# Performance work log

Hardware: AMD Instinct MI355X
Metric: run time of the kernel (lower is better)

## Reference

```python
import jax, jax.numpy as jnp
import numpy as np

NUM_HEADS = 8
EPS = 1e-9


def setup_inputs() -> dict:
    key = jax.random.key(0)
    ks = jax.random.split(key, 8)
    B, N, D = 2, 2048, 512
    s = 1.0 / np.sqrt(D)
    x = jax.random.normal(ks[0], (B, N, D), dtype=jnp.float32)
    adjacency = jax.random.uniform(ks[1], (B, N, N), dtype=jnp.float32)
    # Linear weights stored as (in, out) so application is x @ W + b
    W_q = jax.random.normal(ks[2], (D, D), dtype=jnp.float32) * s
    W_k = jax.random.normal(ks[3], (D, D), dtype=jnp.float32) * s
    W_v = jax.random.normal(ks[4], (D, D), dtype=jnp.float32) * s
    b_q = jnp.zeros((D,), jnp.float32)
    b_k = jnp.zeros((D,), jnp.float32)
    b_v = jnp.zeros((D,), jnp.float32)
    # soul_gate: Linear(2D -> 1); weight stored as flat (2D,), bias scalar
    w_g = jax.random.normal(ks[5], (2 * D,), dtype=jnp.float32) * (1.0 / np.sqrt(2 * D))
    b_g = jnp.zeros((), jnp.float32)
    return {"x": x, "adjacency": adjacency, "W_q": W_q, "b_q": b_q,
            "W_k": W_k, "b_k": b_k, "W_v": W_v, "b_v": b_v,
            "w_g": w_g, "b_g": b_g}


def reference(x, adjacency, W_q, b_q, W_k, b_k, W_v, b_v, w_g, b_g):
    B, N, D = x.shape
    H = NUM_HEADS
    hd = D // H
    Q = (x @ W_q + b_q).reshape(B, N, H, hd)
    K = (x @ W_k + b_k).reshape(B, N, H, hd)
    V = (x @ W_v + b_v).reshape(B, N, H, hd)
    scores = jnp.einsum('bihd,bjhd->bhij', Q, K) / jnp.sqrt(jnp.float32(hd))
    # soul_gate(cat[x_i, x_j]) is linear, so it decomposes exactly:
    # bias[b,i,j] = x[b,i]@w_g[:D] + x[b,j]@w_g[D:] + b_g  (same math, no (B,N,N,2D) tensor)
    a = x @ w_g[:D]          # (B, N) contribution of x_i
    c = x @ w_g[D:]          # (B, N) contribution of x_j
    soul_bias = a[:, :, None] + c[:, None, :] + b_g   # (B, N, N)
    scores = scores + (soul_bias + jnp.log(adjacency + EPS))[:, None, :, :]
    attn = jax.nn.softmax(scores, axis=-1)            # (B, H, N, N)
    out = jnp.einsum('bhij,bjhd->bihd', attn, V).reshape(B, N, D)
    return out + x
```

## Files before the change

kernel.cpp:

```cpp
#include <hip/hip_runtime.h>
#include <hip/hip_bf16.h>

typedef __bf16 bf16x8 __attribute__((ext_vector_type(8)));
typedef float f32x4 __attribute__((ext_vector_type(4)));
typedef unsigned short u16x8 __attribute__((ext_vector_type(8)));

#define LOG2E 1.44269504f

__device__ __forceinline__ unsigned short f2bu(float f) {
    __hip_bfloat16 h = __float2bfloat16(f);
    unsigned short u;
    __builtin_memcpy(&u, &h, 2);
    return u;
}

__device__ __forceinline__ float fexp2(float x) {
#if __has_builtin(__builtin_amdgcn_exp2f)
    return __builtin_amdgcn_exp2f(x);
#else
    return __expf(x * 0.69314718f);
#endif
}

__device__ __forceinline__ float bu2f(unsigned short u) {
    unsigned int v = ((unsigned int)u) << 16;
    float f;
    __builtin_memcpy(&f, &v, 4);
    return f;
}

#define GLDS16(gp, lp) __builtin_amdgcn_global_load_lds( \
    (const __attribute__((address_space(1))) unsigned int*)(gp), \
    (__attribute__((address_space(3))) unsigned int*)(lp), 16, 0, 0)

#define OFF_QS  0u
#define OFF_KB  4194304u
#define OFF_VT  8388608u
#define OFF_CV  12582912u
#define OFF_MP  12648448u
#define OFF_PO  29425664u
#define OFF_PL  37814272u
#define OFF_XB  OFF_MP
#define OFF_WT  (OFF_MP + 4194304u)

__global__ void k_prepwt(const float* __restrict__ x, const float* __restrict__ wg,
                         const float* __restrict__ w0, const float* __restrict__ w1,
                         const float* __restrict__ w2,
                         unsigned short* __restrict__ xb, float* __restrict__ cv2,
                         unsigned short* __restrict__ wt) {
    if (blockIdx.x < 1024) {
        int row = blockIdx.x * 4 + (threadIdx.x >> 6);
        int l = threadIdx.x & 63;
        const float4* xr = reinterpret_cast<const float4*>(x + (size_t)row * 512);
        float4 a = xr[l * 2], b2 = xr[l * 2 + 1];
        ushort4 o0, o1;
        o0.x = f2bu(a.x);  o0.y = f2bu(a.y);  o0.z = f2bu(a.z);  o0.w = f2bu(a.w);
        o1.x = f2bu(b2.x); o1.y = f2bu(b2.y); o1.z = f2bu(b2.z); o1.w = f2bu(b2.w);
        ushort4* dst = reinterpret_cast<ushort4*>(xb + (size_t)row * 512);
        dst[l * 2] = o0; dst[l * 2 + 1] = o1;
        const float4* wr = reinterpret_cast<const float4*>(wg + 512);
        float4 g0 = wr[l * 2], g1 = wr[l * 2 + 1];
        float s = a.x * g0.x + a.y * g0.y + a.z * g0.z + a.w * g0.w
                + b2.x * g1.x + b2.y * g1.y + b2.z * g1.z + b2.w * g1.w;
#pragma unroll
        for (int off = 32; off >= 1; off >>= 1) s += __shfl_xor(s, off, 64);
        if (l == 0) cv2[row] = fexp2((s - 8.0f) * LOG2E);
    } else {
        int bid2 = blockIdx.x - 1024;
        int z = bid2 >> 6, yy = bid2 & 63;
        int k0 = (yy >> 3) * 64, n0 = (yy & 7) * 64;
        const float* W = (z == 0) ? w0 : ((z == 1) ? w1 : w2);
        __shared__ float T[64][65];
        int c = threadIdx.x & 63, r0 = threadIdx.x >> 6;
#pragma unroll
        for (int i = 0; i < 16; i++) { int r = r0 + i * 4; T[r][c] = W[(k0 + r) * 512 + n0 + c]; }
        __syncthreads();
        unsigned short* Wt = wt + z * (512 * 512);
#pragma unroll
        for (int i = 0; i < 16; i++) { int a = r0 + i * 4; Wt[(n0 + a) * 512 + k0 + c] = f2bu(T[c][a]); }
    }
}

__global__ void k_adjp(const float* __restrict__ adj, const float* __restrict__ cv2,
                       unsigned short* __restrict__ mp) {
    int blk = blockIdx.x;
    int bic = blk >> 5, jt = blk & 31;
    int b = bic >> 7, ic = bic & 127;
    int t = threadIdx.x;
    int l = t >> 2, r = t & 3, q = l >> 4, cl = l & 15;
    int row = ic * 16 + q * 4 + r;
    const float* ar = adj + ((size_t)(b * 2048 + row)) * 2048 + jt * 64;
    const float* cb = cv2 + b * 2048 + jt * 64;
    ushort4 o;
    o.x = f2bu((ar[cl]      + 1e-9f) * cb[cl]);
    o.y = f2bu((ar[16 + cl] + 1e-9f) * cb[16 + cl]);
    o.z = f2bu((ar[32 + cl] + 1e-9f) * cb[32 + cl]);
    o.w = f2bu((ar[48 + cl] + 1e-9f) * cb[48 + cl]);
    *reinterpret_cast<ushort4*>(mp + (size_t)bic * 32768 + jt * 1024 + t * 4) = o;
}

__global__ __launch_bounds__(256) void k_gemm(
    const unsigned short* __restrict__ xb, const unsigned short* __restrict__ wt,
    const float* __restrict__ bq, const float* __restrict__ bk, const float* __restrict__ bv,
    unsigned short* __restrict__ Qs, unsigned short* __restrict__ Kb,
    unsigned short* __restrict__ Vt) {
    __shared__ __align__(16) unsigned short As[64 * 32];
    __shared__ __align__(16) unsigned short Bs[128 * 32];
    int z = blockIdx.z;
    const unsigned short* Wt = wt + z * (512 * 512);
    const float* bias = (z == 0) ? bq : ((z == 1) ? bk : bv);
    float scale = (z == 0) ? (0.125f * LOG2E) : 1.0f;
    int m0 = blockIdx.x * 64, n0 = blockIdx.y * 128;
    int tid = threadIdx.x, w = tid >> 6, l = tid & 63;
    int q = l >> 4, cl = l & 15;
    f32x4 acc[8];
#pragma unroll
    for (int nt = 0; nt < 8; nt++)
#pragma unroll
        for (int r = 0; r < 4; r++) acc[nt][r] = 0.f;

    int arow = l >> 2, ach = (l & 3) * 8;
    for (int k0 = 0; k0 < 512; k0 += 32) {
        GLDS16(xb + (size_t)(m0 + w * 16 + arow) * 512 + k0 + ach, As + w * 512);
#pragma unroll
        for (int e = 0; e < 2; e++)
            GLDS16(Wt + (size_t)(n0 + w * 32 + e * 16 + arow) * 512 + k0 + ach, Bs + w * 1024 + e * 512);
        __syncthreads();
        bf16x8 af = *reinterpret_cast<const bf16x8*>(As + (w * 16 + cl) * 32 + q * 8);
#pragma unroll
        for (int nt = 0; nt < 8; nt++) {
            bf16x8 bf = *reinterpret_cast<const bf16x8*>(Bs + (nt * 16 + cl) * 32 + q * 8);
            acc[nt] = __builtin_amdgcn_mfma_f32_16x16x32_bf16(af, bf, acc[nt], 0, 0, 0);
        }
        __syncthreads();
    }
    if (z == 2) {
        int n_ = (m0 + w * 16 + q * 4) & 2047;
        int b_ = (m0 + w * 16) >> 11;
#pragma unroll
        for (int nt = 0; nt < 8; nt++) {
            int col = n0 + nt * 16 + cl;
            int h_ = col >> 6, d_ = col & 63;
            float bv_ = bias[col];
            ushort4 o;
            o.x = f2bu(acc[nt][0] + bv_); o.y = f2bu(acc[nt][1] + bv_);
            o.z = f2bu(acc[nt][2] + bv_); o.w = f2bu(acc[nt][3] + bv_);
            *reinterpret_cast<ushort4*>(Vt + ((size_t)((b_ * 8 + h_) * 64 + d_)) * 2048 + n_) = o;
        }
    } else {
        unsigned short* Cout = (z == 0) ? Qs : Kb;
#pragma unroll
        for (int nt = 0; nt < 8; nt++) {
            int col = n0 + nt * 16 + cl;
            float bv_ = bias[col];
#pragma unroll
            for (int r = 0; r < 4; r++) {
                int row = m0 + w * 16 + q * 4 + r;
                Cout[(size_t)row * 512 + col] = f2bu((acc[nt][r] + bv_) * scale);
            }
        }
    }
}

__global__ __launch_bounds__(256, 2) void k_attn(
    const unsigned short* __restrict__ Qs, const unsigned short* __restrict__ Kb,
    const unsigned short* __restrict__ Vt, const unsigned short* __restrict__ mp,
    unsigned short* __restrict__ PO, float* __restrict__ PL) {
    __shared__ __align__(16) unsigned short Ks[4096];
    __shared__ __align__(16) unsigned short Vs[4096];
    __shared__ __align__(16) unsigned short P[4][32 * 68];
    int bid = blockIdx.x;
    int js = bid & 1, it = (bid >> 1) & 15, b = (bid >> 5) & 1, h = bid >> 6;
    int tid = threadIdx.x, w = tid >> 6, l = tid & 63, q = l >> 4, cl = l & 15;
    int bh = b * 8 + h;
    int rowbase = it * 128 + w * 32;

    bf16x8 qf[2][2];
#pragma unroll
    for (int rc = 0; rc < 2; rc++) {
        const unsigned short* qp = Qs + (size_t)(b * 2048 + rowbase + rc * 16 + cl) * 512 + h * 64 + q * 8;
        qf[rc][0] = *reinterpret_cast<const bf16x8*>(qp);
        qf[rc][1] = *reinterpret_cast<const bf16x8*>(qp + 32);
    }
    f32x4 O[2][4];
    float lsum[2][4];
#pragma unroll
    for (int rc = 0; rc < 2; rc++) {
#pragma unroll
        for (int nt = 0; nt < 4; nt++)
#pragma unroll
            for (int r = 0; r < 4; r++) O[rc][nt][r] = 0.f;
#pragma unroll
        for (int r = 0; r < 4; r++) lsum[rc][r] = 0.f;
    }

    const unsigned short* Kh = Kb + (size_t)b * 2048 * 512 + h * 64;
    const unsigned short* Vh = Vt + ((size_t)bh * 64) * 2048;
    const unsigned short* mb0 = mp + ((size_t)(b * 128 + it * 8 + w * 2 + 0)) * 32768 + l * 16;
    const unsigned short* mb1 = mp + ((size_t)(b * 128 + it * 8 + w * 2 + 1)) * 32768 + l * 16;
    unsigned short* pw = &P[w][0];
    int lrow = l >> 2, lch = (l & 3) * 8;

    for (int t = 0; t < 16; t++) {
        int jb = js * 1024 + t * 64;
        int jt = js * 16 + t;
#pragma unroll
        for (int e = 0; e < 2; e++) {
            int c = w * 2 + e, kk = c >> 2, r16 = (c & 3) * 16;
            GLDS16(Kh + (size_t)(jb + r16 + lrow) * 512 + kk * 32 + lch, Ks + kk * 2048 + r16 * 32);
            GLDS16(Vh + (size_t)(r16 + lrow) * 2048 + jb + kk * 32 + lch, Vs + kk * 2048 + r16 * 32);
        }
        u16x8 mh[2][2];
        mh[0][0] = *reinterpret_cast<const u16x8*>(mb0 + (size_t)jt * 1024);
        mh[0][1] = *reinterpret_cast<const u16x8*>(mb0 + (size_t)jt * 1024 + 8);
        mh[1][0] = *reinterpret_cast<const u16x8*>(mb1 + (size_t)jt * 1024);
        mh[1][1] = *reinterpret_cast<const u16x8*>(mb1 + (size_t)jt * 1024 + 8);
        __syncthreads();
        f32x4 S[2][4];
#pragma unroll
        for (int rc = 0; rc < 2; rc++)
#pragma unroll
            for (int r = 0; r < 4; r++) S[rc][0][r] = S[rc][1][r] = S[rc][2][r] = S[rc][3][r] = 0.f;
#pragma unroll
        for (int nt = 0; nt < 4; nt++) {
            bf16x8 kf0 = *reinterpret_cast<const bf16x8*>(Ks + (16 * nt + cl) * 32 + q * 8);
            bf16x8 kf1 = *reinterpret_cast<const bf16x8*>(Ks + 2048 + (16 * nt + cl) * 32 + q * 8);
#pragma unroll
            for (int rc = 0; rc < 2; rc++) {
                S[rc][nt] = __builtin_amdgcn_mfma_f32_16x16x32_bf16(qf[rc][0], kf0, S[rc][nt], 0, 0, 0);
                S[rc][nt] = __builtin_amdgcn_mfma_f32_16x16x32_bf16(qf[rc][1], kf1, S[rc][nt], 0, 0, 0);
            }
        }
#pragma unroll
        for (int rc = 0; rc < 2; rc++)
#pragma unroll
            for (int r = 0; r < 4; r++)
#pragma unroll
                for (int nt = 0; nt < 4; nt++) {
                    float mv = bu2f((r < 2) ? mh[rc][0][r * 4 + nt] : mh[rc][1][(r & 1) * 4 + nt]);
                    float p = fexp2(S[rc][nt][r]) * mv;
                    lsum[rc][r] += p;
                    pw[(rc * 16 + q * 4 + r) * 68 + 16 * nt + cl] = f2bu(p);
                }
#pragma unroll
        for (int rc = 0; rc < 2; rc++) {
            bf16x8 pf0 = *reinterpret_cast<const bf16x8*>(pw + (rc * 16 + cl) * 68 + q * 8);
            bf16x8 pf1 = *reinterpret_cast<const bf16x8*>(pw + (rc * 16 + cl) * 68 + 32 + q * 8);
#pragma unroll
            for (int nt = 0; nt < 4; nt++) {
                bf16x8 vf0 = *reinterpret_cast<const bf16x8*>(Vs + (16 * nt + cl) * 32 + q * 8);
                bf16x8 vf1 = *reinterpret_cast<const bf16x8*>(Vs + 2048 + (16 * nt + cl) * 32 + q * 8);
                O[rc][nt] = __builtin_amdgcn_mfma_f32_16x16x32_bf16(pf0, vf0, O[rc][nt], 0, 0, 0);
                O[rc][nt] = __builtin_amdgcn_mfma_f32_16x16x32_bf16(pf1, vf1, O[rc][nt], 0, 0, 0);
            }
        }
        __syncthreads();
    }

#pragma unroll
    for (int rc = 0; rc < 2; rc++)
#pragma unroll
        for (int r = 0; r < 4; r++) {
            lsum[rc][r] += __shfl_xor(lsum[rc][r], 1, 64);
            lsum[rc][r] += __shfl_xor(lsum[rc][r], 2, 64);
            lsum[rc][r] += __shfl_xor(lsum[rc][r], 4, 64);
            lsum[rc][r] += __shfl_xor(lsum[rc][r], 8, 64);
        }
#pragma unroll
    for (int rc = 0; rc < 2; rc++) {
        size_t chunk = ((size_t)(bh * 128 + it * 8 + w * 2 + rc)) * 2 + js;
        unsigned short* po = PO + chunk * 1024 + l * 16;
#pragma unroll
        for (int r = 0; r < 4; r++) {
            ushort4 o;
            o.x = f2bu(O[rc][0][r]); o.y = f2bu(O[rc][1][r]);
            o.z = f2bu(O[rc][2][r]); o.w = f2bu(O[rc][3][r]);
            *reinterpret_cast<ushort4*>(po + r * 4) = o;
        }
        if (cl == 0) {
#pragma unroll
            for (int r = 0; r < 4; r++)
                PL[chunk * 16 + q * 4 + r] = lsum[rc][r];
        }
    }
}

__global__ void k_comb(const unsigned short* __restrict__ PO, const float* __restrict__ PL,
                       const float* __restrict__ x, float* __restrict__ out) {
    int blk = blockIdx.x;
    int t64 = blk & 31, bh = blk >> 5;
    int b = bh >> 3, h = bh & 7;
    int t = threadIdx.x;
    int l = t >> 2, r = t & 3, q = l >> 4, cl = l & 15;
#pragma unroll
    for (int w = 0; w < 4; w++) {
        int ic = t64 * 4 + w;
        size_t c0 = ((size_t)(bh * 128 + ic)) * 2;
        ushort4 a = *reinterpret_cast<const ushort4*>(PO + c0 * 1024 + t * 4);
        ushort4 c = *reinterpret_cast<const ushort4*>(PO + (c0 + 1) * 1024 + t * 4);
        float inv = 1.0f / (PL[c0 * 16 + q * 4 + r] + PL[(c0 + 1) * 16 + q * 4 + r]);
        size_t gro = (size_t)(b * 2048 + ic * 16 + q * 4 + r) * 512 + h * 64;
        out[gro + 0 * 16 + cl] = (bu2f(a.x) + bu2f(c.x)) * inv + x[gro + 0 * 16 + cl];
        out[gro + 1 * 16 + cl] = (bu2f(a.y) + bu2f(c.y)) * inv + x[gro + 1 * 16 + cl];
        out[gro + 2 * 16 + cl] = (bu2f(a.z) + bu2f(c.z)) * inv + x[gro + 2 * 16 + cl];
        out[gro + 3 * 16 + cl] = (bu2f(a.w) + bu2f(c.w)) * inv + x[gro + 3 * 16 + cl];
    }
}

extern "C" void kernel_launch(void* const* d_in, const int* in_sizes, int n_in,
                              void* d_out, int out_size, void* d_ws, size_t ws_size,
                              hipStream_t stream) {
    const float* x   = (const float*)d_in[0];
    const float* adj = (const float*)d_in[1];
    const float* Wq  = (const float*)d_in[2];
    const float* bq  = (const float*)d_in[3];
    const float* Wk  = (const float*)d_in[4];
    const float* bk  = (const float*)d_in[5];
    const float* Wv  = (const float*)d_in[6];
    const float* bv  = (const float*)d_in[7];
    const float* wg  = (const float*)d_in[8];
    float* out = (float*)d_out;
    char* ws = (char*)d_ws;
    unsigned short* Qs = (unsigned short*)(ws + OFF_QS);
    unsigned short* Kb = (unsigned short*)(ws + OFF_KB);
    unsigned short* Vt = (unsigned short*)(ws + OFF_VT);
    float* cv2 = (float*)(ws + OFF_CV);
    unsigned short* mpm = (unsigned short*)(ws + OFF_MP);
    unsigned short* PO = (unsigned short*)(ws + OFF_PO);
    float* PL = (float*)(ws + OFF_PL);
    unsigned short* xb = (unsigned short*)(ws + OFF_XB);
    unsigned short* wt = (unsigned short*)(ws + OFF_WT);

    k_prepwt<<<1216, 256, 0, stream>>>(x, wg, Wq, Wk, Wv, xb, cv2, wt);
    k_gemm<<<dim3(64, 4, 3), 256, 0, stream>>>(xb, wt, bq, bk, bv, Qs, Kb, Vt);
    k_adjp<<<8192, 256, 0, stream>>>(adj, cv2, mpm);
    k_attn<<<512, 256, 0, stream>>>(Qs, Kb, Vt, mpm, PO, PL);
    k_comb<<<512, 256, 0, stream>>>(PO, PL, x, out);
}
```

Measured before the change: 168.2 us.

## Fuse GEMM with adjacency prep and drop split-KV combine pass

Merges the adjacency-multiplier preprocessing and the QKV projection GEMM into one launch, with block ranges picking the role. The attention kernel now covers the full key range per block with one 16-row tile per wave, computes S transposed (K·Q), and gets row sums from an MFMA against a ones vector. It writes the normalized output plus residual directly, so the partial-output buffers and the combine kernel go away. The adjacency read is vectorized to float4 with a transposed mask layout. This cuts launches and intermediate traffic, but each block now walks 32 key tiles instead of 16 and holds a smaller per-wave query tile, which may lower K/V reuse.

```diff
diff --git a/kernel.cpp b/kernel.cpp
--- a/kernel.cpp
+++ b/kernel.cpp
@@ -37,11 +37,9 @@
 #define OFF_KB  4194304u
 #define OFF_VT  8388608u
 #define OFF_CV  12582912u
-#define OFF_MP  12648448u
-#define OFF_PO  29425664u
-#define OFF_PL  37814272u
-#define OFF_XB  OFF_MP
-#define OFF_WT  (OFF_MP + 4194304u)
+#define OFF_XB  12599296u
+#define OFF_WT  16793600u
+#define OFF_MQ  18366464u
 
 __global__ void k_prepwt(const float* __restrict__ x, const float* __restrict__ wg,
                          const float* __restrict__ w0, const float* __restrict__ w1,
@@ -81,36 +79,39 @@
     }
 }
 
-__global__ void k_adjp(const float* __restrict__ adj, const float* __restrict__ cv2,
-                       unsigned short* __restrict__ mp) {
-    int blk = blockIdx.x;
-    int bic = blk >> 5, jt = blk & 31;
-    int b = bic >> 7, ic = bic & 127;
-    int t = threadIdx.x;
-    int l = t >> 2, r = t & 3, q = l >> 4, cl = l & 15;
-    int row = ic * 16 + q * 4 + r;
-    const float* ar = adj + ((size_t)(b * 2048 + row)) * 2048 + jt * 64;
-    const float* cb = cv2 + b * 2048 + jt * 64;
-    ushort4 o;
-    o.x = f2bu((ar[cl]      + 1e-9f) * cb[cl]);
-    o.y = f2bu((ar[16 + cl] + 1e-9f) * cb[16 + cl]);
-    o.z = f2bu((ar[32 + cl] + 1e-9f) * cb[32 + cl]);
-    o.w = f2bu((ar[48 + cl] + 1e-9f) * cb[48 + cl]);
-    *reinterpret_cast<ushort4*>(mp + (size_t)bic * 32768 + jt * 1024 + t * 4) = o;
-}
-
-__global__ __launch_bounds__(256) void k_gemm(
+__global__ __launch_bounds__(256) void k_mid(
+    const float* __restrict__ adj, const float* __restrict__ cv2,
+    unsigned short* __restrict__ mq,
     const unsigned short* __restrict__ xb, const unsigned short* __restrict__ wt,
     const float* __restrict__ bq, const float* __restrict__ bk, const float* __restrict__ bv,
     unsigned short* __restrict__ Qs, unsigned short* __restrict__ Kb,
     unsigned short* __restrict__ Vt) {
+    if (blockIdx.x < 8192) {
+        int blk = blockIdx.x;
+        int bic = blk >> 5, jt = blk & 31;
+        int b = bic >> 7, ic = bic & 127;
+        int t = threadIdx.x;
+        int l = t >> 2, mt = t & 3, q = l >> 4, cl = l & 15;
+        int j0 = jt * 64 + 16 * mt + q * 4;
+        const float4 av = *reinterpret_cast<const float4*>(
+            adj + ((size_t)(b * 2048 + ic * 16 + cl)) * 2048 + j0);
+        const float4 cv = *reinterpret_cast<const float4*>(cv2 + b * 2048 + j0);
+        ushort4 o;
+        o.x = f2bu((av.x + 1e-9f) * cv.x);
+        o.y = f2bu((av.y + 1e-9f) * cv.y);
+        o.z = f2bu((av.z + 1e-9f) * cv.z);
+        o.w = f2bu((av.w + 1e-9f) * cv.w);
+        *reinterpret_cast<ushort4*>(mq + (size_t)bic * 32768 + jt * 1024 + l * 16 + mt * 4) = o;
+        return;
+    }
+    int gid = blockIdx.x - 8192;
+    int bx = gid & 63, by = (gid >> 6) & 3, z = gid >> 8;
     __shared__ __align__(16) unsigned short As[64 * 32];
     __shared__ __align__(16) unsigned short Bs[128 * 32];
-    int z = blockIdx.z;
     const unsigned short* Wt = wt + z * (512 * 512);
     const float* bias = (z == 0) ? bq : ((z == 1) ? bk : bv);
     float scale = (z == 0) ? (0.125f * LOG2E) : 1.0f;
-    int m0 = blockIdx.x * 64, n0 = blockIdx.y * 128;
+    int m0 = bx * 64, n0 = by * 128;
     int tid = threadIdx.x, w = tid >> 6, l = tid & 63;
     int q = l >> 4, cl = l & 15;
     f32x4 acc[8];
@@ -118,7 +119,6 @@
     for (int nt = 0; nt < 8; nt++)
 #pragma unroll
         for (int r = 0; r < 4; r++) acc[nt][r] = 0.f;
-
     int arow = l >> 2, ach = (l & 3) * 8;
     for (int k0 = 0; k0 < 512; k0 += 32) {
         GLDS16(xb + (size_t)(m0 + w * 16 + arow) * 512 + k0 + ach, As + w * 512);
@@ -164,146 +164,95 @@
 
 __global__ __launch_bounds__(256, 2) void k_attn(
     const unsigned short* __restrict__ Qs, const unsigned short* __restrict__ Kb,
-    const unsigned short* __restrict__ Vt, const unsigned short* __restrict__ mp,
-    unsigned short* __restrict__ PO, float* __restrict__ PL) {
+    const unsigned short* __restrict__ Vt, const unsigned short* __restrict__ mq,
+    const float* __restrict__ x, float* __restrict__ out) {
     __shared__ __align__(16) unsigned short Ks[4096];
     __shared__ __align__(16) unsigned short Vs[4096];
-    __shared__ __align__(16) unsigned short P[4][32 * 68];
+    __shared__ __align__(16) unsigned short PA[4][16 * 72];
     int bid = blockIdx.x;
-    int js = bid & 1, it = (bid >> 1) & 15, b = (bid >> 5) & 1, h = bid >> 6;
+    int ig = bid >> 4, h = (bid >> 1) & 7, b = bid & 1;
     int tid = threadIdx.x, w = tid >> 6, l = tid & 63, q = l >> 4, cl = l & 15;
-    int bh = b * 8 + h;
-    int rowbase = it * 128 + w * 32;
-
-    bf16x8 qf[2][2];
-#pragma unroll
-    for (int rc = 0; rc < 2; rc++) {
-        const unsigned short* qp = Qs + (size_t)(b * 2048 + rowbase + rc * 16 + cl) * 512 + h * 64 + q * 8;
-        qf[rc][0] = *reinterpret_cast<const bf16x8*>(qp);
-        qf[rc][1] = *reinterpret_cast<const bf16x8*>(qp + 32);
-    }
-    f32x4 O[2][4];
-    float lsum[2][4];
-#pragma unroll
-    for (int rc = 0; rc < 2; rc++) {
-#pragma unroll
-        for (int nt = 0; nt < 4; nt++)
-#pragma unroll
-            for (int r = 0; r < 4; r++) O[rc][nt][r] = 0.f;
-#pragma unroll
-        for (int r = 0; r < 4; r++) lsum[rc][r] = 0.f;
-    }
+    int i0w = ig * 64 + w * 16;
+    int ic = ig * 4 + w;
+
+    bf16x8 qf0, qf1;
+    {
+        const unsigned short* qp = Qs + (size_t)(b * 2048 + i0w + cl) * 512 + h * 64 + q * 8;
+        qf0 = *reinterpret_cast<const bf16x8*>(qp);
+        qf1 = *reinterpret_cast<const bf16x8*>(qp + 32);
+    }
+    bf16x8 ones;
+#pragma unroll
+    for (int i = 0; i < 8; i++) { unsigned short o1 = 0x3F80; __builtin_memcpy(((unsigned short*)&ones) + i, &o1, 2); }
+
+    f32x4 O[4];
+    f32x4 Osum;
+#pragma unroll
+    for (int nt = 0; nt < 4; nt++)
+#pragma unroll
+        for (int r = 0; r < 4; r++) O[nt][r] = 0.f;
+#pragma unroll
+    for (int r = 0; r < 4; r++) Osum[r] = 0.f;
 
     const unsigned short* Kh = Kb + (size_t)b * 2048 * 512 + h * 64;
-    const unsigned short* Vh = Vt + ((size_t)bh * 64) * 2048;
-    const unsigned short* mb0 = mp + ((size_t)(b * 128 + it * 8 + w * 2 + 0)) * 32768 + l * 16;
-    const unsigned short* mb1 = mp + ((size_t)(b * 128 + it * 8 + w * 2 + 1)) * 32768 + l * 16;
-    unsigned short* pw = &P[w][0];
+    const unsigned short* Vh = Vt + ((size_t)(b * 8 + h) * 64) * 2048;
+    const unsigned short* mb = mq + (size_t)(b * 128 + ic) * 32768 + l * 16;
+    unsigned short* pw = &PA[w][0];
     int lrow = l >> 2, lch = (l & 3) * 8;
 
-    for (int t = 0; t < 16; t++) {
-        int jb = js * 1024 + t * 64;
-        int jt = js * 16 + t;
+    for (int t = 0; t < 32; t++) {
+        int jb = t * 64;
 #pragma unroll
         for (int e = 0; e < 2; e++) {
             int c = w * 2 + e, kk = c >> 2, r16 = (c & 3) * 16;
             GLDS16(Kh + (size_t)(jb + r16 + lrow) * 512 + kk * 32 + lch, Ks + kk * 2048 + r16 * 32);
             GLDS16(Vh + (size_t)(r16 + lrow) * 2048 + jb + kk * 32 + lch, Vs + kk * 2048 + r16 * 32);
         }
-        u16x8 mh[2][2];
-        mh[0][0] = *reinterpret_cast<const u16x8*>(mb0 + (size_t)jt * 1024);
-        mh[0][1] = *reinterpret_cast<const u16x8*>(mb0 + (size_t)jt * 1024 + 8);
-        mh[1][0] = *reinterpret_cast<const u16x8*>(mb1 + (size_t)jt * 1024);
-        mh[1][1] = *reinterpret_cast<const u16x8*>(mb1 + (size_t)jt * 1024 + 8);
-        __syncthreads();
-        f32x4 S[2][4];
-#pragma unroll
-        for (int rc = 0; rc < 2; rc++)
-#pragma unroll
-            for (int r = 0; r < 4; r++) S[rc][0][r] = S[rc][1][r] = S[rc][2][r] = S[rc][3][r] = 0.f;
+        u16x8 mh0 = *reinterpret_cast<const u16x8*>(mb + (size_t)t * 1024);
+        u16x8 mh1 = *reinterpret_cast<const u16x8*>(mb + (size_t)t * 1024 + 8);
+        __syncthreads();
+        f32x4 S[4];
+#pragma unroll
+        for (int mt = 0; mt < 4; mt++) {
+#pragma unroll
+            for (int r = 0; r < 4; r++) S[mt][r] = 0.f;
+            bf16x8 kf0 = *reinterpret_cast<const bf16x8*>(Ks + (16 * mt + cl) * 32 + q * 8);
+            bf16x8 kf1 = *reinterpret_cast<const bf16x8*>(Ks + 2048 + (16 * mt + cl) * 32 + q * 8);
+            S[mt] = __builtin_amdgcn_mfma_f32_16x16x32_bf16(kf0, qf0, S[mt], 0, 0, 0);
+            S[mt] = __builtin_amdgcn_mfma_f32_16x16x32_bf16(kf1, qf1, S[mt], 0, 0, 0);
+        }
+#pragma unroll
+        for (int mt = 0; mt < 4; mt++) {
+            float p0 = fexp2(S[mt][0]) * bu2f((mt < 2) ? mh0[mt * 4 + 0] : mh1[(mt - 2) * 4 + 0]);
+            float p1 = fexp2(S[mt][1]) * bu2f((mt < 2) ? mh0[mt * 4 + 1] : mh1[(mt - 2) * 4 + 1]);
+            float p2 = fexp2(S[mt][2]) * bu2f((mt < 2) ? mh0[mt * 4 + 2] : mh1[(mt - 2) * 4 + 2]);
+            float p3 = fexp2(S[mt][3]) * bu2f((mt < 2) ? mh0[mt * 4 + 3] : mh1[(mt - 2) * 4 + 3]);
+            ushort4 o;
+            o.x = f2bu(p0); o.y = f2bu(p1); o.z = f2bu(p2); o.w = f2bu(p3);
+            *reinterpret_cast<ushort4*>(pw + cl * 72 + 16 * mt + q * 4) = o;
+        }
+#pragma unroll
+        for (int jc = 0; jc < 2; jc++) {
+            bf16x8 pf = *reinterpret_cast<const bf16x8*>(pw + cl * 72 + jc * 32 + q * 8);
+#pragma unroll
+            for (int nt = 0; nt < 4; nt++) {
+                bf16x8 vf = *reinterpret_cast<const bf16x8*>(Vs + jc * 2048 + (16 * nt + cl) * 32 + q * 8);
+                O[nt] = __builtin_amdgcn_mfma_f32_16x16x32_bf16(pf, vf, O[nt], 0, 0, 0);
+            }
+            Osum = __builtin_amdgcn_mfma_f32_16x16x32_bf16(pf, ones, Osum, 0, 0, 0);
+        }
+        __syncthreads();
+    }
+
+#pragma unroll
+    for (int r = 0; r < 4; r++) {
+        float inv = 1.0f / Osum[r];
+        size_t base = (size_t)(b * 2048 + i0w + q * 4 + r) * 512 + h * 64;
 #pragma unroll
         for (int nt = 0; nt < 4; nt++) {
-            bf16x8 kf0 = *reinterpret_cast<const bf16x8*>(Ks + (16 * nt + cl) * 32 + q * 8);
-            bf16x8 kf1 = *reinterpret_cast<const bf16x8*>(Ks + 2048 + (16 * nt + cl) * 32 + q * 8);
-#pragma unroll
-            for (int rc = 0; rc < 2; rc++) {
-                S[rc][nt] = __builtin_amdgcn_mfma_f32_16x16x32_bf16(qf[rc][0], kf0, S[rc][nt], 0, 0, 0);
-                S[rc][nt] = __builtin_amdgcn_mfma_f32_16x16x32_bf16(qf[rc][1], kf1, S[rc][nt], 0, 0, 0);
-            }
-        }
-#pragma unroll
-        for (int rc = 0; rc < 2; rc++)
-#pragma unroll
-            for (int r = 0; r < 4; r++)
-#pragma unroll
-                for (int nt = 0; nt < 4; nt++) {
-                    float mv = bu2f((r < 2) ? mh[rc][0][r * 4 + nt] : mh[rc][1][(r & 1) * 4 + nt]);
-                    float p = fexp2(S[rc][nt][r]) * mv;
-                    lsum[rc][r] += p;
-                    pw[(rc * 16 + q * 4 + r) * 68 + 16 * nt + cl] = f2bu(p);
-                }
-#pragma unroll
-        for (int rc = 0; rc < 2; rc++) {
-            bf16x8 pf0 = *reinterpret_cast<const bf16x8*>(pw + (rc * 16 + cl) * 68 + q * 8);
-            bf16x8 pf1 = *reinterpret_cast<const bf16x8*>(pw + (rc * 16 + cl) * 68 + 32 + q * 8);
-#pragma unroll
-            for (int nt = 0; nt < 4; nt++) {
-                bf16x8 vf0 = *reinterpret_cast<const bf16x8*>(Vs + (16 * nt + cl) * 32 + q * 8);
-                bf16x8 vf1 = *reinterpret_cast<const bf16x8*>(Vs + 2048 + (16 * nt + cl) * 32 + q * 8);
-                O[rc][nt] = __builtin_amdgcn_mfma_f32_16x16x32_bf16(pf0, vf0, O[rc][nt], 0, 0, 0);
-                O[rc][nt] = __builtin_amdgcn_mfma_f32_16x16x32_bf16(pf1, vf1, O[rc][nt], 0, 0, 0);
-            }
-        }
-        __syncthreads();
-    }
-
-#pragma unroll
-    for (int rc = 0; rc < 2; rc++)
-#pragma unroll
-        for (int r = 0; r < 4; r++) {
-            lsum[rc][r] += __shfl_xor(lsum[rc][r], 1, 64);
-            lsum[rc][r] += __shfl_xor(lsum[rc][r], 2, 64);
-            lsum[rc][r] += __shfl_xor(lsum[rc][r], 4, 64);
-            lsum[rc][r] += __shfl_xor(lsum[rc][r], 8, 64);
-        }
-#pragma unroll
-    for (int rc = 0; rc < 2; rc++) {
-        size_t chunk = ((size_t)(bh * 128 + it * 8 + w * 2 + rc)) * 2 + js;
-        unsigned short* po = PO + chunk * 1024 + l * 16;
-#pragma unroll
-        for (int r = 0; r < 4; r++) {
-            ushort4 o;
-            o.x = f2bu(O[rc][0][r]); o.y = f2bu(O[rc][1][r]);
-            o.z = f2bu(O[rc][2][r]); o.w = f2bu(O[rc][3][r]);
-            *reinterpret_cast<ushort4*>(po + r * 4) = o;
-        }
-        if (cl == 0) {
-#pragma unroll
-            for (int r = 0; r < 4; r++)
-                PL[chunk * 16 + q * 4 + r] = lsum[rc][r];
-        }
-    }
-}
-
-__global__ void k_comb(const unsigned short* __restrict__ PO, const float* __restrict__ PL,
-                       const float* __restrict__ x, float* __restrict__ out) {
-    int blk = blockIdx.x;
-    int t64 = blk & 31, bh = blk >> 5;
-    int b = bh >> 3, h = bh & 7;
-    int t = threadIdx.x;
-    int l = t >> 2, r = t & 3, q = l >> 4, cl = l & 15;
-#pragma unroll
-    for (int w = 0; w < 4; w++) {
-        int ic = t64 * 4 + w;
-        size_t c0 = ((size_t)(bh * 128 + ic)) * 2;
-        ushort4 a = *reinterpret_cast<const ushort4*>(PO + c0 * 1024 + t * 4);
-        ushort4 c = *reinterpret_cast<const ushort4*>(PO + (c0 + 1) * 1024 + t * 4);
-        float inv = 1.0f / (PL[c0 * 16 + q * 4 + r] + PL[(c0 + 1) * 16 + q * 4 + r]);
-        size_t gro = (size_t)(b * 2048 + ic * 16 + q * 4 + r) * 512 + h * 64;
-        out[gro + 0 * 16 + cl] = (bu2f(a.x) + bu2f(c.x)) * inv + x[gro + 0 * 16 + cl];
-        out[gro + 1 * 16 + cl] = (bu2f(a.y) + bu2f(c.y)) * inv + x[gro + 1 * 16 + cl];
-        out[gro + 2 * 16 + cl] = (bu2f(a.z) + bu2f(c.z)) * inv + x[gro + 2 * 16 + cl];
-        out[gro + 3 * 16 + cl] = (bu2f(a.w) + bu2f(c.w)) * inv + x[gro + 3 * 16 + cl];
+            size_t idx = base + 16 * nt + cl;
+            out[idx] = O[nt][r] * inv + x[idx];
+        }
     }
 }
 
@@ -325,15 +274,11 @@
     unsigned short* Kb = (unsigned short*)(ws + OFF_KB);
     unsigned short* Vt = (unsigned short*)(ws + OFF_VT);
     float* cv2 = (float*)(ws + OFF_CV);
-    unsigned short* mpm = (unsigned short*)(ws + OFF_MP);
-    unsigned short* PO = (unsigned short*)(ws + OFF_PO);
-    float* PL = (float*)(ws + OFF_PL);
     unsigned short* xb = (unsigned short*)(ws + OFF_XB);
     unsigned short* wt = (unsigned short*)(ws + OFF_WT);
+    unsigned short* mqp = (unsigned short*)(ws + OFF_MQ);
 
     k_prepwt<<<1216, 256, 0, stream>>>(x, wg, Wq, Wk, Wv, xb, cv2, wt);
-    k_gemm<<<dim3(64, 4, 3), 256, 0, stream>>>(xb, wt, bq, bk, bv, Qs, Kb, Vt);
-    k_adjp<<<8192, 256, 0, stream>>>(adj, cv2, mpm);
-    k_attn<<<512, 256, 0, stream>>>(Qs, Kb, Vt, mpm, PO, PL);
-    k_comb<<<512, 256, 0, stream>>>(PO, PL, x, out);
-}
+    k_mid<<<8960, 256, 0, stream>>>(adj, cv2, mqp, xb, wt, bq, bk, bv, Qs, Kb, Vt);
+    k_attn<<<512, 256, 0, stream>>>(Qs, Kb, Vt, mqp, x, out);
+}
```

Measured after the change: 159.7 us. 1.05x faster.
